# Kernel tuning notes

Hardware: AMD Instinct MI355X
Metric: run time of the kernel (lower is better)

## Reference

```python
import jax, jax.numpy as jnp
import numpy as np


def maxpool2x2(x):
    # NCHW 2x2 max pool, stride 2
    return jax.lax.reduce_window(x, -jnp.inf, jax.lax.max, (1, 1, 2, 2), (1, 1, 2, 2), 'VALID')


def _xavier_uniform(k, shape):
    fan_out, fan_in = shape
    lim = np.sqrt(6.0 / (fan_in + fan_out))
    return jax.random.uniform(k, shape, jnp.float32, -lim, lim)


def setup_inputs() -> dict:
    key = jax.random.key(0)
    ks = jax.random.split(key, 5)
    C = 64
    x = jax.random.normal(ks[0], (4, C, 128, 128), jnp.float32)
    Wq = _xavier_uniform(ks[1], (C // 8, C))  # 1x1 conv == channel matmul
    Wk = _xavier_uniform(ks[2], (C // 8, C))
    Wv = _xavier_uniform(ks[3], (C // 2, C))
    Wo = _xavier_uniform(ks[4], (C, C // 2))
    gamma = jnp.full((1,), 0.1, jnp.float32)  # nonzero so attention branch contributes
    return {"x": x, "Wq": Wq, "Wk": Wk, "Wv": Wv, "Wo": Wo, "gamma": gamma}


def reference(x, Wq, Wk, Wv, Wo, gamma):
    b, c, w, h = x.shape
    # 1x1 convs as channel contractions
    q = jnp.einsum('oc,bchw->bohw', Wq, x).reshape(b, c // 8, w * h)          # [b, c/8, k]
    k_ = maxpool2x2(jnp.einsum('oc,bchw->bohw', Wk, x)).reshape(b, c // 8, -1)  # [b, c/8, f]
    v = maxpool2x2(jnp.einsum('oc,bchw->bohw', Wv, x)).reshape(b, c // 2, -1)   # [b, c/2, f]
    # softmax over full-resolution query positions k (last axis), per pooled position f
    weights = jax.nn.softmax(jnp.einsum('bcf,bck->bfk', k_, q), axis=-1)        # [b, f, k]
    out = jnp.einsum('bcf,bfk->bck', v, weights).reshape(b, c // 2, w, h)       # [b, c/2, w, h]
    out = jnp.einsum('oc,bchw->bohw', Wo, out)                                   # [b, c, w, h]
    return gamma * out + x
```

## Files before the change

### kernel.cpp

```cpp
#include <hip/hip_runtime.h>
#include <cstdint>
#include <cstddef>


#define LOG2E 1.44269504088896340736f
#define FE_A 8388608.0f
#define FE_B 1064993098.0f

typedef __attribute__((ext_vector_type(8)))  __bf16 bf8_t;
typedef __attribute__((ext_vector_type(16))) float  fx16;

__device__ __forceinline__ unsigned short f2bf(float f) {
  unsigned int u = __builtin_bit_cast(unsigned int, f);
  u += 0x7FFFu + ((u >> 16) & 1u);
  return (unsigned short)(u >> 16);
}
__device__ __forceinline__ float bf2f(unsigned short h) {
  unsigned int u = ((unsigned int)h) << 16;
  return __builtin_bit_cast(float, u);
}
__device__ __forceinline__ unsigned int pk2(unsigned short lo, unsigned short hi) {
  return (unsigned int)lo | ((unsigned int)hi << 16);
}
__device__ __forceinline__ int pi16(int s) {
  int m = (s >> 2) & 3;
  return (m == 1 || m == 2) ? (s ^ 12) : s;
}
__device__ __forceinline__ unsigned fe_u(float s) {
  return (unsigned)fmaf(s, FE_A, FE_B);
}
__device__ __forceinline__ float fe_f(float s) {
  return __builtin_bit_cast(float, fe_u(s));
}
__device__ __forceinline__ unsigned fe_pk(float s0, float s1) {
  return __builtin_amdgcn_perm(fe_u(s1), fe_u(s0), 0x07060302);
}

#define MFMA __builtin_amdgcn_mfma_f32_32x32x16_bf16

__global__ void __launch_bounds__(512) k_qkv(const float* __restrict__ x,
                                             const float* __restrict__ Wq,
                                             const float* __restrict__ Wk,
                                             const float* __restrict__ Wv,
                                             const float* __restrict__ Wo,
                                             unsigned short* __restrict__ Qp,
                                             unsigned short* __restrict__ KpB,
                                             float* __restrict__ Vp,
                                             unsigned short* __restrict__ Wop) {
  if (blockIdx.x == 256) {
    for (int i = threadIdx.x; i < 2048; i += 512) {
      int c = i & 31;
      Wop[i] = f2bf(Wo[(i & ~31) | (c & 16) | pi16(c & 15)]);
    }
    return;
  }
  __shared__ unsigned int xs[256 * 64];
  int t = threadIdx.x;
  int b = blockIdx.x >> 6, T = blockIdx.x & 63;
  {
    int pos = t & 255, cslot = t >> 8;
    const float* xb = x + (size_t)b * (64 * 16384) + T * 256 + pos;
    int sw = pos & 15;
    unsigned int* row = xs + pos * 64;
#pragma unroll
    for (int i = 0; i < 16; ++i) {
      int p = cslot * 16 + i;
      float g0 = xb[(size_t)(2 * p) * 16384];
      float g1 = xb[(size_t)(2 * p + 1) * 16384];
      unsigned short h0 = f2bf(g0), h1 = f2bf(g1);
      unsigned short l0 = f2bf(g0 - bf2f(h0)), l1 = f2bf(g1 - bf2f(h1));
      int q = p >> 2, d = p & 3;
      row[((q + sw) & 15) * 4 + d] = pk2(h0, h1);
      row[((q + 8 + sw) & 15) * 4 + d] = pk2(l0, l1);
    }
  }
  int wv = t >> 6, lane = t & 63;
  int cg = wv & 3, Mt = wv >> 2;
  int m = lane & 31, h = lane >> 5;
  const float* wrow;
  float scale = 1.0f;
  bool zero = false;
  if (Mt == 0) {
    if (m < 8) wrow = Wq + m * 64;
    else if (m < 16) { wrow = Wk + (m - 8) * 64; scale = LOG2E; }
    else wrow = Wv + (m - 16) * 64;
  } else {
    if (m < 16) wrow = Wv + (m + 16) * 64;
    else { wrow = Wq; zero = true; }
  }
  bf8_t Ahi[4], Alo[4];
#pragma unroll
  for (int kk = 0; kk < 4; ++kk) {
    unsigned short hi8[8], lo8[8];
#pragma unroll
    for (int j = 0; j < 8; ++j) {
      float w = zero ? 0.f : wrow[kk * 16 + h * 8 + j] * scale;
      unsigned short wh = f2bf(w);
      hi8[j] = wh;
      lo8[j] = f2bf(w - bf2f(wh));
    }
    uint4 uh, ul;
    uh.x = pk2(hi8[0], hi8[1]); uh.y = pk2(hi8[2], hi8[3]);
    uh.z = pk2(hi8[4], hi8[5]); uh.w = pk2(hi8[6], hi8[7]);
    ul.x = pk2(lo8[0], lo8[1]); ul.y = pk2(lo8[2], lo8[3]);
    ul.z = pk2(lo8[4], lo8[5]); ul.w = pk2(lo8[6], lo8[7]);
    Ahi[kk] = __builtin_bit_cast(bf8_t, uh);
    Alo[kk] = __builtin_bit_cast(bf8_t, ul);
  }
  __syncthreads();
  fx16 z;
#pragma unroll
  for (int i = 0; i < 16; ++i) z[i] = 0.f;
  fx16 D0 = z, D1 = z;
#pragma unroll
  for (int r = 0; r < 2; ++r) {
    fx16 acc = z;
    int pos = cg * 32 + r * 128 + (lane & 31);
    const unsigned int* row = xs + pos * 64;
    int sw = pos & 15;
#pragma unroll
    for (int kk = 0; kk < 4; ++kk) {
      int q = 2 * kk + h;
      bf8_t Bh = *reinterpret_cast<const bf8_t*>(&row[((q + sw) & 15) * 4]);
      bf8_t Bl = *reinterpret_cast<const bf8_t*>(&row[((q + 8 + sw) & 15) * 4]);
      acc = MFMA(Ahi[kk], Bh, acc, 0, 0, 0);
      acc = MFMA(Ahi[kk], Bl, acc, 0, 0, 0);
      acc = MFMA(Alo[kk], Bh, acc, 0, 0, 0);
    }
    if (r == 0) D0 = acc; else D1 = acc;
  }
  uint2 z2; z2.x = z2.y = 0u;
  if (Mt == 0) {
#pragma unroll
    for (int r = 0; r < 2; ++r) {
      const fx16& D = r ? D1 : D0;
      int gpos = T * 256 + r * 128 + cg * 32 + (lane & 31);
      unsigned short* qd = Qp + ((size_t)b * 16384 + gpos) * 16;
      uint2 qa;
      qa.x = pk2(f2bf(D[0]), f2bf(D[1]));
      qa.y = pk2(f2bf(D[2]), f2bf(D[3]));
      *reinterpret_cast<uint2*>(qd + h * 4) = qa;
      *reinterpret_cast<uint2*>(qd + 8 + h * 4) = z2;
    }
  }
  float pm[16];
#pragma unroll
  for (int r0 = 0; r0 < 16; ++r0) {
    float a = fmaxf(D0[r0], __shfl_xor(D0[r0], 1));
    float bb = fmaxf(D1[r0], __shfl_xor(D1[r0], 1));
    pm[r0] = fmaxf(a, bb);
  }
  if ((lane & 1) == 0) {
    size_t idx = (size_t)b * 4096 + T * 64 + cg * 16 + ((lane & 31) >> 1);
    float* vd = Vp + idx * 32;
    if (Mt == 0) {
      uint2 kw;
      kw.x = pk2(f2bf(pm[4]), f2bf(pm[5]));
      kw.y = pk2(f2bf(pm[6]), f2bf(pm[7]));
      *reinterpret_cast<uint2*>(KpB + idx * 16 + h * 4) = kw;
      *reinterpret_cast<float4*>(vd + h * 4) = make_float4(pm[8], pm[9], pm[10], pm[11]);
      *reinterpret_cast<float4*>(vd + 8 + h * 4) = make_float4(pm[12], pm[13], pm[14], pm[15]);
    } else {
      *reinterpret_cast<uint2*>(KpB + idx * 16 + 8 + h * 4) = z2;
      *reinterpret_cast<float4*>(vd + 16 + h * 4) = make_float4(pm[0], pm[1], pm[2], pm[3]);
      *reinterpret_cast<float4*>(vd + 24 + h * 4) = make_float4(pm[4], pm[5], pm[6], pm[7]);
    }
  }
}

__global__ void __launch_bounds__(256, 4) k_lsum(const unsigned short* __restrict__ Qp,
                                                 const unsigned short* __restrict__ KpB,
                                                 float* __restrict__ Lpart) {
  int b = blockIdx.x >> 8, r = blockIdx.x & 255;
  int g = r >> 2, kq = r & 3;
  int wv = threadIdx.x >> 6, lane = threadIdx.x & 63;
  int half = lane >> 5, l31 = lane & 31;
  const unsigned short* kb =
      KpB + ((size_t)(b * 4096 + g * 64 + l31)) * 16 + half * 8;
  bf8_t A0 = *reinterpret_cast<const bf8_t*>(kb);
  bf8_t A1 = *reinterpret_cast<const bf8_t*>(kb + 32 * 16);
  const unsigned short* qbase = Qp + ((size_t)b * 16384) * 16 + half * 8;
  fx16 z;
#pragma unroll
  for (int i = 0; i < 16; ++i) z[i] = 0.f;
  float l[32];
#pragma unroll
  for (int i = 0; i < 32; ++i) l[i] = 0.f;
  int t0 = kq * 128 + wv * 32;
  bf8_t B = *reinterpret_cast<const bf8_t*>(qbase + (size_t)(t0 * 32 + l31) * 16);
  for (int i = 0; i < 32; ++i) {
    int tn = t0 + ((i + 1) & 31);
    bf8_t nB = *reinterpret_cast<const bf8_t*>(qbase + (size_t)(tn * 32 + l31) * 16);
    fx16 s0 = MFMA(A0, B, z, 0, 0, 0);
    fx16 s1 = MFMA(A1, B, z, 0, 0, 0);
#pragma unroll
    for (int r0 = 0; r0 < 16; ++r0) l[r0] += fe_f(s0[r0]);
#pragma unroll
    for (int r0 = 0; r0 < 16; ++r0) l[16 + r0] += fe_f(s1[r0]);
    B = nB;
  }
#pragma unroll
  for (int r0 = 0; r0 < 32; ++r0)
    for (int d = 1; d < 32; d <<= 1) l[r0] += __shfl_xor(l[r0], d);
  __shared__ float sl[4][2][32];
  if (l31 == 0) {
#pragma unroll
    for (int r0 = 0; r0 < 16; ++r0) {
      int row = (r0 & 3) + 8 * (r0 >> 2) + 4 * half;
      sl[wv][0][row] = l[r0];
      sl[wv][1][row] = l[16 + r0];
    }
  }
  __syncthreads();
  if (threadIdx.x < 64) {
    int fgi = threadIdx.x >> 5, row = threadIdx.x & 31;
    float L = sl[0][fgi][row] + sl[1][fgi][row] + sl[2][fgi][row] + sl[3][fgi][row];
    Lpart[(size_t)kq * 16384 + b * 4096 + g * 64 + fgi * 32 + row] = L;
  }
}

__global__ void __launch_bounds__(256) k_pack(const float* __restrict__ Vp,
                                              const float* __restrict__ Lpart,
                                              unsigned short* __restrict__ Vpp) {
  int b = blockIdx.x >> 4, f0 = (blockIdx.x & 15) * 256;
  __shared__ unsigned short Tt[32][264];
  int t = threadIdx.x;
  size_t li = (size_t)b * 4096 + f0 + t;
  float L = Lpart[li] + Lpart[li + 16384] + Lpart[li + 32768] + Lpart[li + 49152];
  float rl = 1.0f / L;
  const float* vp = Vp + li * 32;
  int fl = (t & ~15) | pi16(t & 15);
  for (int c = 0; c < 32; ++c) Tt[c][fl] = f2bf(vp[c] * rl);
  __syncthreads();
  for (int u = t; u < 1024; u += 256) {
    int row = u >> 5, e0 = (u & 31) * 8;
    uint4 val = *reinterpret_cast<const uint4*>(&Tt[row][e0]);
    *reinterpret_cast<uint4*>(Vpp + ((size_t)b * 32 + row) * 4096 + f0 + e0) = val;
  }
}

__global__ void __launch_bounds__(256, 4) k_attn(const unsigned short* __restrict__ Qp,
                                                 const unsigned short* __restrict__ KpB,
                                                 const unsigned short* __restrict__ Vpp,
                                                 const unsigned short* __restrict__ Wop,
                                                 const float* __restrict__ x,
                                                 const float* __restrict__ gamma,
                                                 float* __restrict__ out) {
  int b = blockIdx.x >> 8, kp = blockIdx.x & 255;
  int wv = threadIdx.x >> 6, lane = threadIdx.x & 63;
  int half = lane >> 5, l31 = lane & 31;
  int kbase = kp * 64;
  const unsigned short* qb = Qp + ((size_t)b * 16384 + kbase + l31) * 16 + half * 8;
  bf8_t Bq0 = *reinterpret_cast<const bf8_t*>(qb);
  bf8_t Bq1 = *reinterpret_cast<const bf8_t*>(qb + 32 * 16);
  fx16 z;
#pragma unroll
  for (int i = 0; i < 16; ++i) z[i] = 0.f;
  fx16 acc0 = z, acc1 = z;
  const unsigned short* kpB = KpB + ((size_t)b * 4096 + l31) * 16 + half * 8;
  const unsigned short* vpB = Vpp + ((size_t)(b * 32 + l31)) * 4096 + half * 8;
  int c0 = wv * 32;
  int f0 = c0 * 32;
  bf8_t Ak  = *reinterpret_cast<const bf8_t*>(kpB + (size_t)f0 * 16);
  bf8_t Av0 = *reinterpret_cast<const bf8_t*>(vpB + f0);
  bf8_t Av1 = *reinterpret_cast<const bf8_t*>(vpB + f0 + 16);
  for (int fc = 0; fc < 32; ++fc) {
    int f1 = (c0 + ((fc + 1) & 31)) * 32;
    bf8_t nAk  = *reinterpret_cast<const bf8_t*>(kpB + (size_t)f1 * 16);
    bf8_t nAv0 = *reinterpret_cast<const bf8_t*>(vpB + f1);
    bf8_t nAv1 = *reinterpret_cast<const bf8_t*>(vpB + f1 + 16);
    fx16 s0 = MFMA(Ak, Bq0, z, 0, 0, 0);
    fx16 s1 = MFMA(Ak, Bq1, z, 0, 0, 0);
    uint4 u00, u01, u10, u11;
    u00.x = fe_pk(s0[0], s0[1]);   u00.y = fe_pk(s0[2], s0[3]);
    u00.z = fe_pk(s0[4], s0[5]);   u00.w = fe_pk(s0[6], s0[7]);
    u01.x = fe_pk(s0[8], s0[9]);   u01.y = fe_pk(s0[10], s0[11]);
    u01.z = fe_pk(s0[12], s0[13]); u01.w = fe_pk(s0[14], s0[15]);
    u10.x = fe_pk(s1[0], s1[1]);   u10.y = fe_pk(s1[2], s1[3]);
    u10.z = fe_pk(s1[4], s1[5]);   u10.w = fe_pk(s1[6], s1[7]);
    u11.x = fe_pk(s1[8], s1[9]);   u11.y = fe_pk(s1[10], s1[11]);
    u11.z = fe_pk(s1[12], s1[13]); u11.w = fe_pk(s1[14], s1[15]);
    bf8_t P00 = __builtin_bit_cast(bf8_t, u00);
    bf8_t P01 = __builtin_bit_cast(bf8_t, u01);
    bf8_t P10 = __builtin_bit_cast(bf8_t, u10);
    bf8_t P11 = __builtin_bit_cast(bf8_t, u11);
    acc0 = MFMA(Av0, P00, acc0, 0, 0, 0);
    acc1 = MFMA(Av0, P10, acc1, 0, 0, 0);
    acc0 = MFMA(Av1, P01, acc0, 0, 0, 0);
    acc1 = MFMA(Av1, P11, acc1, 0, 0, 0);
    Ak = nAk; Av0 = nAv0; Av1 = nAv1;
  }
  __shared__ float sacc[4][2][4][64][4];
#pragma unroll
  for (int j4 = 0; j4 < 4; ++j4) {
    *reinterpret_cast<float4*>(&sacc[wv][0][j4][lane][0]) =
        make_float4(acc0[4 * j4], acc0[4 * j4 + 1], acc0[4 * j4 + 2], acc0[4 * j4 + 3]);
    *reinterpret_cast<float4*>(&sacc[wv][1][j4][lane][0]) =
        make_float4(acc1[4 * j4], acc1[4 * j4 + 1], acc1[4 * j4 + 2], acc1[4 * j4 + 3]);
  }
  __syncthreads();
  if (wv >= 2) return;
  int kt = wv;
  int k = kbase + kt * 32 + l31;
  const float* xp = x + (size_t)b * 64 * 16384 + k;
  float xv0[16], xv1[16];
#pragma unroll
  for (int r0 = 0; r0 < 16; ++r0) {
    int row = (r0 & 3) + 8 * (r0 >> 2) + 4 * half;
    xv0[r0] = xp[(size_t)row * 16384];
    xv1[r0] = xp[(size_t)(row + 32) * 16384];
  }
  fx16 tot;
#pragma unroll
  for (int j4 = 0; j4 < 4; ++j4) {
    float4 a0 = *reinterpret_cast<const float4*>(&sacc[0][kt][j4][lane][0]);
    float4 a1 = *reinterpret_cast<const float4*>(&sacc[1][kt][j4][lane][0]);
    float4 a2 = *reinterpret_cast<const float4*>(&sacc[2][kt][j4][lane][0]);
    float4 a3 = *reinterpret_cast<const float4*>(&sacc[3][kt][j4][lane][0]);
    tot[4 * j4]     = (a0.x + a1.x) + (a2.x + a3.x);
    tot[4 * j4 + 1] = (a0.y + a1.y) + (a2.y + a3.y);
    tot[4 * j4 + 2] = (a0.z + a1.z) + (a2.z + a3.z);
    tot[4 * j4 + 3] = (a0.w + a1.w) + (a2.w + a3.w);
  }
  bf8_t Ob0, Ob1;
#pragma unroll
  for (int j = 0; j < 8; ++j) { Ob0[j] = (__bf16)tot[j]; Ob1[j] = (__bf16)tot[8 + j]; }
  const unsigned short* wb = Wop + l31 * 32 + half * 8;
  bf8_t Aw00 = *reinterpret_cast<const bf8_t*>(wb);
  bf8_t Aw01 = *reinterpret_cast<const bf8_t*>(wb + 16);
  bf8_t Aw10 = *reinterpret_cast<const bf8_t*>(wb + 1024);
  bf8_t Aw11 = *reinterpret_cast<const bf8_t*>(wb + 1024 + 16);
  fx16 y0 = MFMA(Aw00, Ob0, z, 0, 0, 0);
  y0 = MFMA(Aw01, Ob1, y0, 0, 0, 0);
  fx16 y1 = MFMA(Aw10, Ob0, z, 0, 0, 0);
  y1 = MFMA(Aw11, Ob1, y1, 0, 0, 0);
  float g = gamma[0];
  float* op = out + (size_t)b * 64 * 16384 + k;
#pragma unroll
  for (int r0 = 0; r0 < 16; ++r0) {
    int row = (r0 & 3) + 8 * (r0 >> 2) + 4 * half;
    op[(size_t)row * 16384]        = fmaf(g, y0[r0], xv0[r0]);
    op[(size_t)(row + 32) * 16384] = fmaf(g, y1[r0], xv1[r0]);
  }
}

extern "C" void kernel_launch(void* const* d_in, const int* in_sizes, int n_in,
                              void* d_out, int out_size, void* d_ws, size_t ws_size,
                              hipStream_t stream) {
  const float* x     = (const float*)d_in[0];
  const float* Wq    = (const float*)d_in[1];
  const float* Wk    = (const float*)d_in[2];
  const float* Wv    = (const float*)d_in[3];
  const float* Wo    = (const float*)d_in[4];
  const float* gamma = (const float*)d_in[5];
  float* out = (float*)d_out;
  char* ws = (char*)d_ws;
  unsigned short* Qp    = (unsigned short*)(ws + 0);
  unsigned short* KpB   = (unsigned short*)(ws + 2097152);
  float*          Vp    = (float*)(ws + 2621440);
  unsigned short* Vpp   = (unsigned short*)(ws + 4718592);
  float*          Lpart = (float*)(ws + 5767168);
  unsigned short* Wop   = (unsigned short*)(ws + 6029312);

  k_qkv <<<dim3(257),  dim3(512), 0, stream>>>(x, Wq, Wk, Wv, Wo, Qp, KpB, Vp, Wop);
  k_lsum<<<dim3(1024), dim3(256), 0, stream>>>(Qp, KpB, Lpart);
  k_pack<<<dim3(64),   dim3(256), 0, stream>>>(Vp, Lpart, Vpp);
  k_attn<<<dim3(1024), dim3(256), 0, stream>>>(Qp, KpB, Vpp, Wop, x, gamma, out);
}
```

Baseline: 154.4 us.

## Split qkv blocks, shrink lsum to single-wave blocks, software-pipeline MFMA loops

k_qkv now runs 512 blocks of 256 threads, each handling half of a 256-position tile, which gives more parallelism and uses less LDS per block. k_lsum becomes one-wave blocks over 16 key slices that write partial sums straight to Lpart with no LDS reduction, so k_pack sums 16 partials instead of 4. The score MFMA in both k_lsum and k_attn is software-pipelined one iteration ahead so the exp/pack work overlaps the next MFMA, with loads prefetched two steps ahead. k_attn's occupancy hint drops from 4 to 3 to leave room for the extra live registers. The costs are a larger Lpart buffer (Wop moved to a new offset) and more global partial-sum traffic.

```diff
diff --git a/kernel.cpp b/kernel.cpp
--- a/kernel.cpp
+++ b/kernel.cpp
@@ -38,7 +38,7 @@
 
 #define MFMA __builtin_amdgcn_mfma_f32_32x32x16_bf16
 
-__global__ void __launch_bounds__(512) k_qkv(const float* __restrict__ x,
+__global__ void __launch_bounds__(256) k_qkv(const float* __restrict__ x,
                                              const float* __restrict__ Wq,
                                              const float* __restrict__ Wk,
                                              const float* __restrict__ Wv,
@@ -47,19 +47,22 @@
                                              unsigned short* __restrict__ KpB,
                                              float* __restrict__ Vp,
                                              unsigned short* __restrict__ Wop) {
-  if (blockIdx.x == 256) {
-    for (int i = threadIdx.x; i < 2048; i += 512) {
+  if (blockIdx.x == 512) {
+    for (int i = threadIdx.x; i < 2048; i += 256) {
       int c = i & 31;
       Wop[i] = f2bf(Wo[(i & ~31) | (c & 16) | pi16(c & 15)]);
     }
     return;
   }
-  __shared__ unsigned int xs[256 * 64];
+  __shared__ unsigned int xs[128 * 64];
   int t = threadIdx.x;
-  int b = blockIdx.x >> 6, T = blockIdx.x & 63;
+  int b = blockIdx.x >> 7, rr = blockIdx.x & 127;
+  int T = rr >> 1, ph = rr & 1;
   {
-    int pos = t & 255, cslot = t >> 8;
-    const float* xb = x + (size_t)b * (64 * 16384) + T * 256 + pos;
+    int pos = t & 127, cslot = t >> 7;
+    int r = pos >> 6, c = pos & 63;
+    const float* xb =
+        x + (size_t)b * (64 * 16384) + T * 256 + r * 128 + ph * 64 + c;
     int sw = pos & 15;
     unsigned int* row = xs + pos * 64;
 #pragma unroll
@@ -75,7 +78,7 @@
     }
   }
   int wv = t >> 6, lane = t & 63;
-  int cg = wv & 3, Mt = wv >> 2;
+  int cg = wv & 1, Mt = wv >> 1;
   int m = lane & 31, h = lane >> 5;
   const float* wrow;
   float scale = 1.0f;
@@ -115,7 +118,7 @@
 #pragma unroll
   for (int r = 0; r < 2; ++r) {
     fx16 acc = z;
-    int pos = cg * 32 + r * 128 + (lane & 31);
+    int pos = r * 64 + cg * 32 + (lane & 31);
     const unsigned int* row = xs + pos * 64;
     int sw = pos & 15;
 #pragma unroll
@@ -134,7 +137,7 @@
 #pragma unroll
     for (int r = 0; r < 2; ++r) {
       const fx16& D = r ? D1 : D0;
-      int gpos = T * 256 + r * 128 + cg * 32 + (lane & 31);
+      int gpos = T * 256 + r * 128 + ph * 64 + cg * 32 + (lane & 31);
       unsigned short* qd = Qp + ((size_t)b * 16384 + gpos) * 16;
       uint2 qa;
       qa.x = pk2(f2bf(D[0]), f2bf(D[1]));
@@ -151,7 +154,8 @@
     pm[r0] = fmaxf(a, bb);
   }
   if ((lane & 1) == 0) {
-    size_t idx = (size_t)b * 4096 + T * 64 + cg * 16 + ((lane & 31) >> 1);
+    int cell = ph * 32 + cg * 16 + ((lane & 31) >> 1);
+    size_t idx = (size_t)b * 4096 + T * 64 + cell;
     float* vd = Vp + idx * 32;
     if (Mt == 0) {
       uint2 kw;
@@ -168,15 +172,14 @@
   }
 }
 
-__global__ void __launch_bounds__(256, 4) k_lsum(const unsigned short* __restrict__ Qp,
-                                                 const unsigned short* __restrict__ KpB,
-                                                 float* __restrict__ Lpart) {
-  int b = blockIdx.x >> 8, r = blockIdx.x & 255;
-  int g = r >> 2, kq = r & 3;
-  int wv = threadIdx.x >> 6, lane = threadIdx.x & 63;
+__global__ void __launch_bounds__(64, 4) k_lsum(const unsigned short* __restrict__ Qp,
+                                                const unsigned short* __restrict__ KpB,
+                                                float* __restrict__ Lpart) {
+  int b = blockIdx.x >> 10, gp = (blockIdx.x >> 4) & 63, ks = blockIdx.x & 15;
+  int lane = threadIdx.x & 63;
   int half = lane >> 5, l31 = lane & 31;
   const unsigned short* kb =
-      KpB + ((size_t)(b * 4096 + g * 64 + l31)) * 16 + half * 8;
+      KpB + ((size_t)(b * 4096 + gp * 64 + l31)) * 16 + half * 8;
   bf8_t A0 = *reinterpret_cast<const bf8_t*>(kb);
   bf8_t A1 = *reinterpret_cast<const bf8_t*>(kb + 32 * 16);
   const unsigned short* qbase = Qp + ((size_t)b * 16384) * 16 + half * 8;
@@ -186,36 +189,37 @@
   float l[32];
 #pragma unroll
   for (int i = 0; i < 32; ++i) l[i] = 0.f;
-  int t0 = kq * 128 + wv * 32;
-  bf8_t B = *reinterpret_cast<const bf8_t*>(qbase + (size_t)(t0 * 32 + l31) * 16);
+  int t0 = ks * 32;
+#define QLD(j) (*reinterpret_cast<const bf8_t*>( \
+    qbase + (size_t)(((t0 + ((j) & 31)) * 32 + l31)) * 16))
+  bf8_t Bc = QLD(0);
+  fx16 sp0 = MFMA(A0, Bc, z, 0, 0, 0);
+  fx16 sp1 = MFMA(A1, Bc, z, 0, 0, 0);
+  Bc = QLD(1);
+  bf8_t Bn = QLD(2);
   for (int i = 0; i < 32; ++i) {
-    int tn = t0 + ((i + 1) & 31);
-    bf8_t nB = *reinterpret_cast<const bf8_t*>(qbase + (size_t)(tn * 32 + l31) * 16);
-    fx16 s0 = MFMA(A0, B, z, 0, 0, 0);
-    fx16 s1 = MFMA(A1, B, z, 0, 0, 0);
-#pragma unroll
-    for (int r0 = 0; r0 < 16; ++r0) l[r0] += fe_f(s0[r0]);
-#pragma unroll
-    for (int r0 = 0; r0 < 16; ++r0) l[16 + r0] += fe_f(s1[r0]);
-    B = nB;
-  }
+    fx16 sn0 = MFMA(A0, Bc, z, 0, 0, 0);
+    fx16 sn1 = MFMA(A1, Bc, z, 0, 0, 0);
+#pragma unroll
+    for (int r0 = 0; r0 < 16; ++r0) l[r0] += fe_f(sp0[r0]);
+#pragma unroll
+    for (int r0 = 0; r0 < 16; ++r0) l[16 + r0] += fe_f(sp1[r0]);
+    sp0 = sn0; sp1 = sn1;
+    Bc = Bn;
+    Bn = QLD(i + 3);
+  }
+#undef QLD
 #pragma unroll
   for (int r0 = 0; r0 < 32; ++r0)
     for (int d = 1; d < 32; d <<= 1) l[r0] += __shfl_xor(l[r0], d);
-  __shared__ float sl[4][2][32];
   if (l31 == 0) {
+    size_t base = (size_t)ks * 16384 + b * 4096 + gp * 64;
 #pragma unroll
     for (int r0 = 0; r0 < 16; ++r0) {
       int row = (r0 & 3) + 8 * (r0 >> 2) + 4 * half;
-      sl[wv][0][row] = l[r0];
-      sl[wv][1][row] = l[16 + r0];
-    }
-  }
-  __syncthreads();
-  if (threadIdx.x < 64) {
-    int fgi = threadIdx.x >> 5, row = threadIdx.x & 31;
-    float L = sl[0][fgi][row] + sl[1][fgi][row] + sl[2][fgi][row] + sl[3][fgi][row];
-    Lpart[(size_t)kq * 16384 + b * 4096 + g * 64 + fgi * 32 + row] = L;
+      Lpart[base + row] = l[r0];
+      Lpart[base + 32 + row] = l[16 + r0];
+    }
   }
 }
 
@@ -226,7 +230,9 @@
   __shared__ unsigned short Tt[32][264];
   int t = threadIdx.x;
   size_t li = (size_t)b * 4096 + f0 + t;
-  float L = Lpart[li] + Lpart[li + 16384] + Lpart[li + 32768] + Lpart[li + 49152];
+  float L = 0.f;
+#pragma unroll
+  for (int p = 0; p < 16; ++p) L += Lpart[(size_t)p * 16384 + li];
   float rl = 1.0f / L;
   const float* vp = Vp + li * 32;
   int fl = (t & ~15) | pi16(t & 15);
@@ -239,7 +245,7 @@
   }
 }
 
-__global__ void __launch_bounds__(256, 4) k_attn(const unsigned short* __restrict__ Qp,
+__global__ void __launch_bounds__(256, 3) k_attn(const unsigned short* __restrict__ Qp,
                                                  const unsigned short* __restrict__ KpB,
                                                  const unsigned short* __restrict__ Vpp,
                                                  const unsigned short* __restrict__ Wop,
@@ -260,36 +266,39 @@
   const unsigned short* kpB = KpB + ((size_t)b * 4096 + l31) * 16 + half * 8;
   const unsigned short* vpB = Vpp + ((size_t)(b * 32 + l31)) * 4096 + half * 8;
   int c0 = wv * 32;
-  int f0 = c0 * 32;
-  bf8_t Ak  = *reinterpret_cast<const bf8_t*>(kpB + (size_t)f0 * 16);
-  bf8_t Av0 = *reinterpret_cast<const bf8_t*>(vpB + f0);
-  bf8_t Av1 = *reinterpret_cast<const bf8_t*>(vpB + f0 + 16);
+#define KLD(j) (*reinterpret_cast<const bf8_t*>(kpB + (size_t)((c0 + ((j) & 31)) * 32) * 16))
+#define VLD(j, o) (*reinterpret_cast<const bf8_t*>(vpB + (c0 + ((j) & 31)) * 32 + (o)))
+  bf8_t Akc = KLD(0);
+  bf8_t Av0c = VLD(0, 0), Av1c = VLD(0, 16);
+  fx16 sp0 = MFMA(Akc, Bq0, z, 0, 0, 0);
+  fx16 sp1 = MFMA(Akc, Bq1, z, 0, 0, 0);
+  Akc = KLD(1);
+  bf8_t Av0n = VLD(1, 0), Av1n = VLD(1, 16);
+  bf8_t Akin = KLD(2);
   for (int fc = 0; fc < 32; ++fc) {
-    int f1 = (c0 + ((fc + 1) & 31)) * 32;
-    bf8_t nAk  = *reinterpret_cast<const bf8_t*>(kpB + (size_t)f1 * 16);
-    bf8_t nAv0 = *reinterpret_cast<const bf8_t*>(vpB + f1);
-    bf8_t nAv1 = *reinterpret_cast<const bf8_t*>(vpB + f1 + 16);
-    fx16 s0 = MFMA(Ak, Bq0, z, 0, 0, 0);
-    fx16 s1 = MFMA(Ak, Bq1, z, 0, 0, 0);
-    uint4 u00, u01, u10, u11;
-    u00.x = fe_pk(s0[0], s0[1]);   u00.y = fe_pk(s0[2], s0[3]);
-    u00.z = fe_pk(s0[4], s0[5]);   u00.w = fe_pk(s0[6], s0[7]);
-    u01.x = fe_pk(s0[8], s0[9]);   u01.y = fe_pk(s0[10], s0[11]);
-    u01.z = fe_pk(s0[12], s0[13]); u01.w = fe_pk(s0[14], s0[15]);
-    u10.x = fe_pk(s1[0], s1[1]);   u10.y = fe_pk(s1[2], s1[3]);
-    u10.z = fe_pk(s1[4], s1[5]);   u10.w = fe_pk(s1[6], s1[7]);
-    u11.x = fe_pk(s1[8], s1[9]);   u11.y = fe_pk(s1[10], s1[11]);
-    u11.z = fe_pk(s1[12], s1[13]); u11.w = fe_pk(s1[14], s1[15]);
-    bf8_t P00 = __builtin_bit_cast(bf8_t, u00);
-    bf8_t P01 = __builtin_bit_cast(bf8_t, u01);
-    bf8_t P10 = __builtin_bit_cast(bf8_t, u10);
-    bf8_t P11 = __builtin_bit_cast(bf8_t, u11);
-    acc0 = MFMA(Av0, P00, acc0, 0, 0, 0);
-    acc1 = MFMA(Av0, P10, acc1, 0, 0, 0);
-    acc0 = MFMA(Av1, P01, acc0, 0, 0, 0);
-    acc1 = MFMA(Av1, P11, acc1, 0, 0, 0);
-    Ak = nAk; Av0 = nAv0; Av1 = nAv1;
-  }
+    fx16 sn0 = MFMA(Akc, Bq0, z, 0, 0, 0);
+    uint4 u00, u01;
+    u00.x = fe_pk(sp0[0], sp0[1]);   u00.y = fe_pk(sp0[2], sp0[3]);
+    u00.z = fe_pk(sp0[4], sp0[5]);   u00.w = fe_pk(sp0[6], sp0[7]);
+    u01.x = fe_pk(sp0[8], sp0[9]);   u01.y = fe_pk(sp0[10], sp0[11]);
+    u01.z = fe_pk(sp0[12], sp0[13]); u01.w = fe_pk(sp0[14], sp0[15]);
+    acc0 = MFMA(Av0c, __builtin_bit_cast(bf8_t, u00), acc0, 0, 0, 0);
+    acc0 = MFMA(Av1c, __builtin_bit_cast(bf8_t, u01), acc0, 0, 0, 0);
+    fx16 sn1 = MFMA(Akc, Bq1, z, 0, 0, 0);
+    uint4 u10, u11;
+    u10.x = fe_pk(sp1[0], sp1[1]);   u10.y = fe_pk(sp1[2], sp1[3]);
+    u10.z = fe_pk(sp1[4], sp1[5]);   u10.w = fe_pk(sp1[6], sp1[7]);
+    u11.x = fe_pk(sp1[8], sp1[9]);   u11.y = fe_pk(sp1[10], sp1[11]);
+    u11.z = fe_pk(sp1[12], sp1[13]); u11.w = fe_pk(sp1[14], sp1[15]);
+    acc1 = MFMA(Av0c, __builtin_bit_cast(bf8_t, u10), acc1, 0, 0, 0);
+    acc1 = MFMA(Av1c, __builtin_bit_cast(bf8_t, u11), acc1, 0, 0, 0);
+    sp0 = sn0; sp1 = sn1;
+    Akc = Akin; Av0c = Av0n; Av1c = Av1n;
+    Akin = KLD(fc + 3);
+    Av0n = VLD(fc + 2, 0); Av1n = VLD(fc + 2, 16);
+  }
+#undef KLD
+#undef VLD
   __shared__ float sacc[4][2][4][64][4];
 #pragma unroll
   for (int j4 = 0; j4 < 4; ++j4) {
@@ -360,10 +369,10 @@
   float*          Vp    = (float*)(ws + 2621440);
   unsigned short* Vpp   = (unsigned short*)(ws + 4718592);
   float*          Lpart = (float*)(ws + 5767168);
-  unsigned short* Wop   = (unsigned short*)(ws + 6029312);
-
-  k_qkv <<<dim3(257),  dim3(512), 0, stream>>>(x, Wq, Wk, Wv, Wo, Qp, KpB, Vp, Wop);
-  k_lsum<<<dim3(1024), dim3(256), 0, stream>>>(Qp, KpB, Lpart);
+  unsigned short* Wop   = (unsigned short*)(ws + 6815744);
+
+  k_qkv <<<dim3(513),  dim3(256), 0, stream>>>(x, Wq, Wk, Wv, Wo, Qp, KpB, Vp, Wop);
+  k_lsum<<<dim3(4096), dim3(64),  0, stream>>>(Qp, KpB, Lpart);
   k_pack<<<dim3(64),   dim3(256), 0, stream>>>(Vp, Lpart, Vpp);
   k_attn<<<dim3(1024), dim3(256), 0, stream>>>(Qp, KpB, Vpp, Wop, x, gamma, out);
 }
```

New measurement: 157.4 us. Within noise of the previous version (+1.9%).
